# Kernel optimization log

Measured on AMD Instinct MI355X. Metric: run time of the kernel, lower is better.

Reference implementation:

```python
import jax, jax.numpy as jnp
import numpy as np

N, E, G = 25000, 400000, 8
D = 128  # node/edge/global feature width
CONCAT = 4 * D  # send + recv + edge + repeated-global


def _dense(k, fan_in, fan_out):
    kw, kb = jax.random.split(k)
    scale = 1.0 / np.sqrt(fan_in)
    W = jax.random.uniform(kw, (fan_in, fan_out), jnp.float32, -scale, scale)
    b = jax.random.uniform(kb, (fan_out,), jnp.float32, -scale, scale)
    return W, b


def setup_inputs() -> dict:
    key = jax.random.key(0)
    ks = jax.random.split(key, 16)
    nodes = jax.random.normal(ks[0], (N, D), jnp.float32)
    edges = jax.random.normal(ks[1], (E, D), jnp.float32)
    glbs = jax.random.normal(ks[2], (G, D), jnp.float32)
    senders = jax.random.randint(ks[3], (E,), 0, N, jnp.int32)
    receivers = jax.random.randint(ks[4], (E,), 0, N, jnp.int32)
    n_node = jnp.full((G,), N // G, jnp.int32)
    n_edge = jnpip = jnp.full((G,), E // G, jnp.int32)
    # node MLP [CONCAT -> 256 -> 128]
    Wn0, bn0 = _dense(ks[5], CONCAT, 256)
    Wn1, bn1 = _dense(ks[6], 256, 128)
    # edge MLP [CONCAT -> 256 -> 128]
    We0, be0 = _dense(ks[7], CONCAT, 256)
    We1, be1 = _dense(ks[8], 256, 128)
    # global MLPs [D -> 128] each, final [384 -> 128]
    Wgn, bgn = _dense(ks[9], D, 128)
    Wge, bge = _dense(ks[10], D, 128)
    Wg, bg = _dense(ks[11], D, 128)
    Wf, bf = _dense(ks[12], 3 * 128, 128)
    return dict(nodes=nodes, edges=edges, glbs=glbs, senders=senders,
                receivers=receivers, n_node=n_node, n_edge=n_edge,
                Wn0=Wn0, bn0=bn0, Wn1=Wn1, bn1=bn1,
                We0=We0, be0=be0, We1=We1, be1=be1,
                Wgn=Wgn, bgn=bgn, Wge=Wge, bge=bge,
                Wg=Wg, bg=bg, Wf=Wf, bf=bf)


def reference(nodes, edges, glbs, senders, receivers, n_node, n_edge,
              Wn0, bn0, Wn1, bn1, We0, be0, We1, be1,
              Wgn, bgn, Wge, bge, Wg, bg, Wf, bf):
    act = jax.nn.leaky_relu  # default negative_slope=0.01, dropout is identity

    def mlp2(x, W0, b0, W1, b1):
        return act(act(x @ W0 + b0) @ W1 + b1)

    def mlp1(x, W, b):
        return act(x @ W + b)

    # gather + concat: [E, 4D]
    edge_glb = jnp.repeat(glbs, n_edge, axis=0, total_repeat_length=E)
    concat = jnp.concatenate([nodes[senders], nodes[receivers], edges, edge_glb], axis=1)

    # per-edge node-message MLP, scatter-sum to receivers
    msgs = mlp2(concat, Wn0, bn0, Wn1, bn1)            # [E, 128]
    new_nodes = jax.ops.segment_sum(msgs, receivers, num_segments=N)

    # per-edge edge-update MLP
    new_edges = mlp2(concat, We0, be0, We1, be1)       # [E, 128]

    # per-graph sums of node/edge features (== split_and_sum)
    gid_n = jnp.repeat(jnp.arange(G), n_node, total_repeat_length=N)
    gid_e = jnp.repeat(jnp.arange(G), n_edge, total_repeat_length=E)
    sum_nodes = jax.ops.segment_sum(nodes, gid_n, num_segments=G)  # [G, D]
    sum_edges = jax.ops.segment_sum(edges, gid_e, num_segments=G)  # [G, D]

    tmp_g = mlp1(glbs, Wg, bg)
    tmp_n = mlp1(sum_nodes, Wgn, bgn)
    tmp_e = mlp1(sum_edges, Wge, bge)
    new_global = mlp1(jnp.concatenate([tmp_g, tmp_n, tmp_e], axis=1), Wf, bf)

    return new_nodes, new_edges, new_global
```

## Files before the change

kernel.cpp:

```cpp
#include <hip/hip_runtime.h>
#include <hip/hip_bf16.h>

#define D_ 128

typedef __attribute__((ext_vector_type(8))) short short8;
typedef __attribute__((ext_vector_type(4))) float f32x4;
typedef __attribute__((address_space(1))) const unsigned int g_u32;
typedef __attribute__((address_space(3))) unsigned int l_u32;

static __device__ __forceinline__ float lrelu(float x) { return x > 0.f ? x : 0.01f * x; }
static __device__ __forceinline__ short f2bf(float f) {
    __hip_bfloat16 h = __float2bfloat16(f);
    return *reinterpret_cast<short*>(&h);
}
static __device__ __forceinline__ unsigned short f2bfu(float f) {
    __hip_bfloat16 h = __float2bfloat16(f);
    return *reinterpret_cast<unsigned short*>(&h);
}
static __device__ __forceinline__ unsigned int f2fp8x4(float a, float b, float c, float d) {
    unsigned int p = __builtin_amdgcn_cvt_pk_fp8_f32(a, b, 0, 0);
    p = __builtin_amdgcn_cvt_pk_fp8_f32(c, d, p, 1);
    return p;
}

__global__ void prep(const float* __restrict__ Wn0, const float* __restrict__ We0,
                     const float* __restrict__ Wn1, const float* __restrict__ We1,
                     const float* __restrict__ bn0, const float* __restrict__ be0,
                     const float* __restrict__ bn1, const float* __restrict__ be1,
                     const float* __restrict__ nodes, const float* __restrict__ glbs,
                     long nq,
                     unsigned char* __restrict__ W0F, short* __restrict__ W1T,
                     float* __restrict__ b0c, float* __restrict__ b1c,
                     unsigned char* __restrict__ nodes_f8, unsigned char* __restrict__ glbs_f8) {
    long i = (long)blockIdx.x * 256 + threadIdx.x;
    if (i < nq) {
        float4 v = ((const float4*)nodes)[i];
        ((unsigned int*)nodes_f8)[i] = f2fp8x4(v.x, v.y, v.z, v.w);
        return;
    }
    long j = i - nq;
    if (j < 512 * 128) {
        int n = (int)(j >> 7), k4 = (int)(j & 127);
        float v0, v1, v2, v3;
        if (n < 256) {
            v0 = Wn0[(k4 * 4 + 0) * 256 + n]; v1 = Wn0[(k4 * 4 + 1) * 256 + n];
            v2 = Wn0[(k4 * 4 + 2) * 256 + n]; v3 = Wn0[(k4 * 4 + 3) * 256 + n];
        } else {
            int m = n - 256;
            v0 = We0[(k4 * 4 + 0) * 256 + m]; v1 = We0[(k4 * 4 + 1) * 256 + m];
            v2 = We0[(k4 * 4 + 2) * 256 + m]; v3 = We0[(k4 * 4 + 3) * 256 + m];
        }
        ((unsigned int*)W0F)[n * 128 + k4] = f2fp8x4(v0, v1, v2, v3);
        return;
    }
    j -= 512 * 128;
    if (j < 256 * 256) {
        int n = (int)(j >> 8), k = (int)(j & 255);
        float v = (n < 128) ? Wn1[k * 128 + n] : We1[k * 128 + (n - 128)];
        W1T[j] = f2bf(v);
        return;
    }
    j -= 256 * 256;
    if (j < 512) { b0c[j] = (j < 256) ? bn0[j] : be0[j - 256]; return; }
    if (j < 768) { int t = (int)j - 512; b1c[t] = (t < 128) ? bn1[t] : be1[t - 128]; return; }
    j -= 768;
    if (j < 256) {
        const float* g4 = glbs + j * 4;
        ((unsigned int*)glbs_f8)[j] = f2fp8x4(g4[0], g4[1], g4[2], g4[3]);
    }
}

__global__ void hist_recv(const int* __restrict__ receivers, int E_, int* __restrict__ cnt) {
    int e = blockIdx.x * 256 + threadIdx.x;
    if (e < E_) atomicAdd(&cnt[receivers[e]], 1);
}

__global__ void scan_counts(const int* __restrict__ cnt, int N_, int* __restrict__ off) {
    __shared__ int part[256];
    int t = threadIdx.x;
    int chunk = (N_ + 255) / 256;
    int b = t * chunk, e = min(N_, b + chunk);
    int s = 0;
    for (int i = b; i < e; i++) s += cnt[i];
    part[t] = s;
    __syncthreads();
    for (int o = 1; o < 256; o <<= 1) {
        int v = (t >= o) ? part[t - o] : 0;
        __syncthreads();
        part[t] += v;
        __syncthreads();
    }
    int run = part[t] - s;
    for (int i = b; i < e; i++) { off[i] = run; run += cnt[i]; }
}

__global__ void place_edges(const int* __restrict__ receivers, int E_,
                            int* __restrict__ off, int* __restrict__ sorted) {
    int e = blockIdx.x * 256 + threadIdx.x;
    if (e < E_) {
        int p = atomicAdd(&off[receivers[e]], 1);
        sorted[p] = e;
    }
}

__global__ void seg_sum(const float* __restrict__ src, const int* __restrict__ counts,
                        int G, int rows, int chunk, float* __restrict__ out) {
    int c4 = threadIdx.x & 31;
    int rl = threadIdx.x >> 5;
    int r0 = blockIdx.x * chunk + rl;
    int rend = min(rows, blockIdx.x * chunk + chunk);
    int s_ = 0;
    int cu0 = 0x7fffffff, cu1 = 0x7fffffff, cu2 = 0x7fffffff, cu3 = 0x7fffffff;
    int cu4 = 0x7fffffff, cu5 = 0x7fffffff, cu6 = 0x7fffffff, cu7 = 0x7fffffff;
#define CUF(I, CU) if (I < G) { s_ += counts[I]; CU = s_; }
    CUF(0, cu0) CUF(1, cu1) CUF(2, cu2) CUF(3, cu3)
    CUF(4, cu4) CUF(5, cu5) CUF(6, cu6) CUF(7, cu7)
#undef CUF
    f32x4 acc = {0.f, 0.f, 0.f, 0.f};
    int accg = -1;
    for (int r = r0; r < rend; r += 8) {
        int g = (r >= cu0) + (r >= cu1) + (r >= cu2) + (r >= cu3)
              + (r >= cu4) + (r >= cu5) + (r >= cu6) + (r >= cu7);
        if (g != accg) {
            if (accg >= 0) {
#pragma unroll
                for (int j = 0; j < 4; j++) atomicAdd(&out[accg * D_ + c4 * 4 + j], acc[j]);
            }
            acc = (f32x4){0.f, 0.f, 0.f, 0.f}; accg = g;
        }
        const float4 v = *(const float4*)(src + (long)r * D_ + c4 * 4);
        acc[0] += v.x; acc[1] += v.y; acc[2] += v.z; acc[3] += v.w;
    }
    if (accg >= 0) {
#pragma unroll
        for (int j = 0; j < 4; j++) atomicAdd(&out[accg * D_ + c4 * 4 + j], acc[j]);
    }
}

__global__ void conv_sum_edges(const float* __restrict__ src, const int* __restrict__ counts,
                               int G, int rows, int chunk,
                               float* __restrict__ out, unsigned char* __restrict__ dst_f8) {
    int c4 = threadIdx.x & 31;
    int rl = threadIdx.x >> 5;
    int r0 = blockIdx.x * chunk + rl;
    int rend = min(rows, blockIdx.x * chunk + chunk);
    int s_ = 0;
    int cu0 = 0x7fffffff, cu1 = 0x7fffffff, cu2 = 0x7fffffff, cu3 = 0x7fffffff;
    int cu4 = 0x7fffffff, cu5 = 0x7fffffff, cu6 = 0x7fffffff, cu7 = 0x7fffffff;
#define CUF(I, CU) if (I < G) { s_ += counts[I]; CU = s_; }
    CUF(0, cu0) CUF(1, cu1) CUF(2, cu2) CUF(3, cu3)
    CUF(4, cu4) CUF(5, cu5) CUF(6, cu6) CUF(7, cu7)
#undef CUF
    f32x4 acc = {0.f, 0.f, 0.f, 0.f};
    int accg = -1;
    for (int r = r0; r < rend; r += 8) {
        int g = (r >= cu0) + (r >= cu1) + (r >= cu2) + (r >= cu3)
              + (r >= cu4) + (r >= cu5) + (r >= cu6) + (r >= cu7);
        if (g != accg) {
            if (accg >= 0) {
#pragma unroll
                for (int j = 0; j < 4; j++) atomicAdd(&out[accg * D_ + c4 * 4 + j], acc[j]);
            }
            acc = (f32x4){0.f, 0.f, 0.f, 0.f}; accg = g;
        }
        const float4 v = *(const float4*)(src + (long)r * D_ + c4 * 4);
        acc[0] += v.x; acc[1] += v.y; acc[2] += v.z; acc[3] += v.w;
        ((unsigned int*)dst_f8)[(long)r * 32 + c4] = f2fp8x4(v.x, v.y, v.z, v.w);
    }
    if (accg >= 0) {
#pragma unroll
        for (int j = 0; j < 4; j++) atomicAdd(&out[accg * D_ + c4 * 4 + j], acc[j]);
    }
}

__global__ void global_mlp(const float* __restrict__ glbs, const float* __restrict__ sumn,
                           const float* __restrict__ sume,
                           const float* __restrict__ Wg, const float* __restrict__ bg,
                           const float* __restrict__ Wgn, const float* __restrict__ bgn,
                           const float* __restrict__ Wge, const float* __restrict__ bge,
                           const float* __restrict__ Wf, const float* __restrict__ bfv,
                           float* __restrict__ outg) {
    __shared__ float s_tmp[384];
    int r = blockIdx.x;
    int c = threadIdx.x;
    float a0 = 0.f, a1 = 0.f, a2 = 0.f;
    for (int k = 0; k < 128; k++) {
        a0 += glbs[r * 128 + k] * Wg[k * 128 + c];
        a1 += sumn[r * 128 + k] * Wgn[k * 128 + c];
        a2 += sume[r * 128 + k] * Wge[k * 128 + c];
    }
    s_tmp[c]       = lrelu(a0 + bg[c]);
    s_tmp[128 + c] = lrelu(a1 + bgn[c]);
    s_tmp[256 + c] = lrelu(a2 + bge[c]);
    __syncthreads();
    float a = 0.f;
    for (int k = 0; k < 384; k++) a += s_tmp[k] * Wf[k * 128 + c];
    outg[r * 128 + c] = lrelu(a + bfv[c]);
}

__launch_bounds__(512, 4)
__global__ void edge_mlp(const unsigned char* __restrict__ nodes_f8,
                         const unsigned char* __restrict__ edges_f8,
                         const unsigned char* __restrict__ glbs_f8,
                         const int* __restrict__ senders, const int* __restrict__ receivers,
                         const int* __restrict__ sorted_eid,
                         const int* __restrict__ n_edge, int G, int NT,
                         const unsigned char* __restrict__ W0F, const short* __restrict__ W1T,
                         const float* __restrict__ b0c, const float* __restrict__ b1c,
                         float* __restrict__ out_nodes, float* __restrict__ out_edges) {
    __shared__ __align__(16) char sX[65536];
    __shared__ int s_eid[64], s_recv[64], s_snd[64], s_gid[64];

    const int tid  = threadIdx.x;
    const int lane = tid & 63;
    const int wid  = tid >> 6;
    const int wn   = wid;
    const int l15  = lane & 15;
    const int lk   = lane >> 4;

    const int tile = blockIdx.x;
    const int base = tile * 64;

    int s_ = 0;
    int cu0 = 0x7fffffff, cu1 = 0x7fffffff, cu2 = 0x7fffffff, cu3 = 0x7fffffff;
    int cu4 = 0x7fffffff, cu5 = 0x7fffffff, cu6 = 0x7fffffff, cu7 = 0x7fffffff;
#define CUF(I, CU) if (I < G) { s_ += n_edge[I]; CU = s_; }
    CUF(0, cu0) CUF(1, cu1) CUF(2, cu2) CUF(3, cu3)
    CUF(4, cu4) CUF(5, cu5) CUF(6, cu6) CUF(7, cu7)
#undef CUF

    if (tid < 64) {
        int eid = sorted_eid[base + tid];
        s_eid[tid]  = eid;
        s_snd[tid]  = senders[eid];
        s_recv[tid] = receivers[eid];
        s_gid[tid]  = (eid >= cu0) + (eid >= cu1) + (eid >= cu2) + (eid >= cu3)
                    + (eid >= cu4) + (eid >= cu5) + (eid >= cu6) + (eid >= cu7);
    }
    __syncthreads();

#pragma unroll
    for (int r = 0; r < 4; ++r) {
        const int p   = r * 8 + wid;
        const int row = 2 * p + (lane >> 5);
        const int src = (lane >> 3) & 3;
        const int sub = lane & 7;
        char* dst = sX + p * 1024;
        const unsigned char* bp = (src == 0) ? nodes_f8 + (long)s_snd[row] * 128
                                 : (src == 1) ? nodes_f8 + (long)s_recv[row] * 128
                                 : (src == 2) ? edges_f8 + (long)s_eid[row] * 128
                                              : glbs_f8 + (long)s_gid[row] * 128;
        __builtin_amdgcn_global_load_lds((g_u32*)(bp + ((sub ^ (row & 7)) << 4)), (l_u32*)dst, 16, 0, 0);
    }
    __syncthreads();

    {
        f32x4 acc[4][2];
#pragma unroll
        for (int mt = 0; mt < 4; ++mt)
#pragma unroll
            for (int nt = 0; nt < 2; ++nt) acc[mt][nt] = (f32x4){0.f, 0.f, 0.f, 0.f};

#pragma unroll
        for (int t = 0; t < 16; ++t) {
            long bfr[2];
#pragma unroll
            for (int nt = 0; nt < 2; ++nt) {
                int n = wn * 32 + nt * 16 + l15;
                bfr[nt] = *(const long*)(W0F + (long)n * 512 + t * 32 + lk * 8);
            }
#pragma unroll
            for (int mt = 0; mt < 4; ++mt) {
                int row = mt * 16 + l15;
                int g16 = (t * 2 + (lk >> 1)) ^ (row & 7);
                long af = *(const long*)(sX + row * 512 + (g16 << 4) + ((lk & 1) << 3));
#pragma unroll
                for (int nt = 0; nt < 2; ++nt)
                    acc[mt][nt] = __builtin_amdgcn_mfma_f32_16x16x32_fp8_fp8(af, bfr[nt], acc[mt][nt], 0, 0, 0);
            }
        }
#pragma unroll
        for (int nt = 0; nt < 2; ++nt) {
            int col = wn * 32 + nt * 16 + l15;
            float bias = b0c[col];
#pragma unroll
            for (int mt = 0; mt < 4; ++mt) {
#pragma unroll
                for (int q = 0; q < 4; ++q) {
                    int row = mt * 16 + lk * 4 + q;
                    float v = lrelu(acc[mt][nt][q] + bias);
                    *(short*)(sX + 32768 + row * 512 + ((col * 2) ^ ((row & 7) << 4))) = f2bf(v);
                }
            }
        }
    }

    {
        f32x4 acc[4][2];
#pragma unroll
        for (int mt = 0; mt < 4; ++mt)
#pragma unroll
            for (int nt = 0; nt < 2; ++nt) acc[mt][nt] = (f32x4){0.f, 0.f, 0.f, 0.f};

#pragma unroll
        for (int t = 0; t < 16; ++t) {
            long bfr[2];
#pragma unroll
            for (int nt = 0; nt < 2; ++nt) {
                int n = 256 + wn * 32 + nt * 16 + l15;
                bfr[nt] = *(const long*)(W0F + (long)n * 512 + t * 32 + lk * 8);
            }
#pragma unroll
            for (int mt = 0; mt < 4; ++mt) {
                int row = mt * 16 + l15;
                int g16 = (t * 2 + (lk >> 1)) ^ (row & 7);
                long af = *(const long*)(sX + row * 512 + (g16 << 4) + ((lk & 1) << 3));
#pragma unroll
                for (int nt = 0; nt < 2; ++nt)
                    acc[mt][nt] = __builtin_amdgcn_mfma_f32_16x16x32_fp8_fp8(af, bfr[nt], acc[mt][nt], 0, 0, 0);
            }
        }
        __syncthreads();
#pragma unroll
        for (int nt = 0; nt < 2; ++nt) {
            int col = wn * 32 + nt * 16 + l15;
            float bias = b0c[256 + col];
#pragma unroll
            for (int mt = 0; mt < 4; ++mt) {
#pragma unroll
                for (int q = 0; q < 4; ++q) {
                    int row = mt * 16 + lk * 4 + q;
                    float v = lrelu(acc[mt][nt][q] + bias);
                    *(short*)(sX + row * 512 + ((col * 2) ^ ((row & 7) << 4))) = f2bf(v);
                }
            }
        }
    }
    __syncthreads();

    const int branch = wid >> 2;
    const int qn     = wid & 3;
    const int hreg   = branch ? 0 : 32768;
    f32x4 acc2[4][2];
#pragma unroll
    for (int mt = 0; mt < 4; ++mt)
#pragma unroll
        for (int nt = 0; nt < 2; ++nt) acc2[mt][nt] = (f32x4){0.f, 0.f, 0.f, 0.f};

#pragma unroll
    for (int kt = 0; kt < 8; ++kt) {
        short8 bfr2[2];
#pragma unroll
        for (int nt = 0; nt < 2; ++nt) {
            int ncl = qn * 32 + nt * 16 + l15;
            bfr2[nt] = *(const short8*)(W1T + (long)(branch * 128 + ncl) * 256 + kt * 32 + lk * 8);
        }
#pragma unroll
        for (int mt = 0; mt < 4; ++mt) {
            int row = mt * 16 + l15;
            int kbyte = kt * 64 + lk * 16;
            short8 af = *(const short8*)(sX + hreg + row * 512 + (kbyte ^ ((row & 7) << 4)));
#pragma unroll
            for (int nt = 0; nt < 2; ++nt)
                acc2[mt][nt] = __builtin_amdgcn_mfma_f32_16x16x32_bf16(af, bfr2[nt], acc2[mt][nt], 0, 0, 0);
        }
    }
    __syncthreads();

#pragma unroll
    for (int nt = 0; nt < 2; ++nt) {
        int ncl = qn * 32 + nt * 16 + l15;
        float bias = b1c[branch * 128 + ncl];
#pragma unroll
        for (int mt = 0; mt < 4; ++mt) {
#pragma unroll
            for (int q = 0; q < 4; ++q) {
                int row = mt * 16 + lk * 4 + q;
                float v = lrelu(acc2[mt][nt][q] + bias);
                if (branch == 0) {
                    *(float*)(sX + 32768 + row * 512 + ((ncl * 4) ^ (((row >> 2) & 3) << 6))) = v;
                } else {
                    out_edges[(long)s_eid[row] * D_ + ncl] = v;
                }
            }
        }
    }
    __syncthreads();

    {
        int c  = tid & 127;
        int qr = tid >> 7;
        int r0 = qr * 16;
        float v[16];
#pragma unroll
        for (int i = 0; i < 16; ++i) {
            int r = r0 + i;
            v[i] = *(const float*)(sX + 32768 + r * 512 + ((c * 4) ^ (((r >> 2) & 3) << 6)));
        }
        float acc_s = 0.f;
        int cur = s_recv[r0];
#pragma unroll
        for (int i = 0; i < 16; ++i) {
            int rc = s_recv[r0 + i];
            if (rc != cur) {
                atomicAdd(&out_nodes[(long)cur * D_ + c], acc_s);
                acc_s = 0.f; cur = rc;
            }
            acc_s += v[i];
        }
        atomicAdd(&out_nodes[(long)cur * D_ + c], acc_s);
    }
}

extern "C" void kernel_launch(void* const* d_in, const int* in_sizes, int n_in,
                              void* d_out, int out_size, void* d_ws, size_t ws_size,
                              hipStream_t stream) {
    const float* nodes     = (const float*)d_in[0];
    const float* edges     = (const float*)d_in[1];
    const float* glbs      = (const float*)d_in[2];
    const int*   senders   = (const int*)d_in[3];
    const int*   receivers = (const int*)d_in[4];
    const int*   n_node    = (const int*)d_in[5];
    const int*   n_edge    = (const int*)d_in[6];
    const float* Wn0 = (const float*)d_in[7];
    const float* bn0 = (const float*)d_in[8];
    const float* Wn1 = (const float*)d_in[9];
    const float* bn1 = (const float*)d_in[10];
    const float* We0 = (const float*)d_in[11];
    const float* be0 = (const float*)d_in[12];
    const float* We1 = (const float*)d_in[13];
    const float* be1 = (const float*)d_in[14];
    const float* Wgn = (const float*)d_in[15];
    const float* bgn = (const float*)d_in[16];
    const float* Wge = (const float*)d_in[17];
    const float* bge = (const float*)d_in[18];
    const float* Wg  = (const float*)d_in[19];
    const float* bg  = (const float*)d_in[20];
    const float* Wf  = (const float*)d_in[21];
    const float* bfv = (const float*)d_in[22];

    const int N = in_sizes[0] / 128;
    const int E = in_sizes[1] / 128;
    const int G = in_sizes[2] / 128;
    const int NT = E / 64;

    char* ws = (char*)d_ws;
    unsigned char* W0F = (unsigned char*)(ws);
    short* W1T  = (short*)(ws + 262144);
    float* b0c  = (float*)(ws + 393216);
    float* b1c  = (float*)(ws + 395264);
    float* sumn = (float*)(ws + 396288);
    float* sume = (float*)(ws + 400384);
    unsigned char* glbs_f8  = (unsigned char*)(ws + 404480);
    unsigned char* nodes_f8 = (unsigned char*)(ws + 405504);
    char* ws2 = ws + 405504 + (size_t)N * 128;
    int* cnt        = (int*)(ws2);
    int* tmp_off    = (int*)(ws2 + (size_t)N * 4);
    int* sorted_eid = (int*)(ws2 + (size_t)N * 8);
    unsigned char* edges_f8 = (unsigned char*)(ws2 + (size_t)N * 8 + (size_t)E * 4);

    float* out_nodes = (float*)d_out;
    float* out_edges = out_nodes + (long)N * 128;
    float* out_glb   = out_edges + (long)E * 128;

    hipMemsetAsync(out_nodes, 0, (size_t)N * 128 * sizeof(float), stream);
    hipMemsetAsync(sumn, 0, 8192, stream);
    hipMemsetAsync(cnt, 0, (size_t)N * 4, stream);

    const long nq = (long)N * 32;
    const long prep_items = nq + 512 * 128 + 256 * 256 + 768 + 256;
    prep<<<(int)((prep_items + 255) / 256), 256, 0, stream>>>(
        Wn0, We0, Wn1, We1, bn0, be0, bn1, be1, nodes, glbs, nq,
        W0F, W1T, b0c, b1c, nodes_f8, glbs_f8);

    hist_recv<<<(E + 255) / 256, 256, 0, stream>>>(receivers, E, cnt);
    scan_counts<<<1, 256, 0, stream>>>(cnt, N, tmp_off);
    place_edges<<<(E + 255) / 256, 256, 0, stream>>>(receivers, E, tmp_off, sorted_eid);

    conv_sum_edges<<<(E + 511) / 512, 256, 0, stream>>>(edges, n_edge, G, E, 512, sume, edges_f8);

    edge_mlp<<<NT, 512, 0, stream>>>(nodes_f8, edges_f8, glbs_f8, senders, receivers,
                                     sorted_eid, n_edge, G, NT,
                                     W0F, W1T, b0c, b1c, out_nodes, out_edges);

    seg_sum<<<(N + 127) / 128, 256, 0, stream>>>(nodes, n_node, G, N, 128, sumn);

    global_mlp<<<G, 128, 0, stream>>>(glbs, sumn, sume, Wg, bg, Wgn, bgn, Wge, bge, Wf, bfv,
                                      out_glb);
}
```

Measured before the change: 919.5 us.

## Fuse receiver histogram into edge conversion, use plain stores for owned segments, widen global MLP

Folds the receiver histogram atomics into the conv_sum_edges pass and drops the separate hist_recv launch. In edge_mlp, a receiver segment that lies wholly inside one thread's 16-row range now gets a plain store instead of an atomicAdd; neighbouring receivers are checked through shared values for the previous and next tile. global_mlp now runs its three small input MLPs in parallel on 384 threads. The plain-store path depends on out_nodes being zero-initialised and on receivers being sorted, so each receiver is fully owned by one range.

```diff
diff --git a/kernel.cpp b/kernel.cpp
--- a/kernel.cpp
+++ b/kernel.cpp
@@ -68,11 +68,6 @@
         const float* g4 = glbs + j * 4;
         ((unsigned int*)glbs_f8)[j] = f2fp8x4(g4[0], g4[1], g4[2], g4[3]);
     }
-}
-
-__global__ void hist_recv(const int* __restrict__ receivers, int E_, int* __restrict__ cnt) {
-    int e = blockIdx.x * 256 + threadIdx.x;
-    if (e < E_) atomicAdd(&cnt[receivers[e]], 1);
 }
 
 __global__ void scan_counts(const int* __restrict__ cnt, int N_, int* __restrict__ off) {
@@ -138,6 +133,7 @@
 }
 
 __global__ void conv_sum_edges(const float* __restrict__ src, const int* __restrict__ counts,
+                               const int* __restrict__ receivers, int* __restrict__ hist,
                                int G, int rows, int chunk,
                                float* __restrict__ out, unsigned char* __restrict__ dst_f8) {
     int c4 = threadIdx.x & 31;
@@ -166,6 +162,7 @@
         const float4 v = *(const float4*)(src + (long)r * D_ + c4 * 4);
         acc[0] += v.x; acc[1] += v.y; acc[2] += v.z; acc[3] += v.w;
         ((unsigned int*)dst_f8)[(long)r * 32 + c4] = f2fp8x4(v.x, v.y, v.z, v.w);
+        if (c4 == 0) atomicAdd(&hist[receivers[r]], 1);
     }
     if (accg >= 0) {
 #pragma unroll
@@ -182,20 +179,20 @@
                            float* __restrict__ outg) {
     __shared__ float s_tmp[384];
     int r = blockIdx.x;
-    int c = threadIdx.x;
-    float a0 = 0.f, a1 = 0.f, a2 = 0.f;
-    for (int k = 0; k < 128; k++) {
-        a0 += glbs[r * 128 + k] * Wg[k * 128 + c];
-        a1 += sumn[r * 128 + k] * Wgn[k * 128 + c];
-        a2 += sume[r * 128 + k] * Wge[k * 128 + c];
-    }
-    s_tmp[c]       = lrelu(a0 + bg[c]);
-    s_tmp[128 + c] = lrelu(a1 + bgn[c]);
-    s_tmp[256 + c] = lrelu(a2 + bge[c]);
-    __syncthreads();
+    int c   = threadIdx.x & 127;
+    int grp = threadIdx.x >> 7;
+    const float* src = (grp == 0) ? glbs : (grp == 1) ? sumn : sume;
+    const float* W   = (grp == 0) ? Wg   : (grp == 1) ? Wgn  : Wge;
+    const float* b   = (grp == 0) ? bg   : (grp == 1) ? bgn  : bge;
     float a = 0.f;
-    for (int k = 0; k < 384; k++) a += s_tmp[k] * Wf[k * 128 + c];
-    outg[r * 128 + c] = lrelu(a + bfv[c]);
+    for (int k = 0; k < 128; k++) a += src[r * 128 + k] * W[k * 128 + c];
+    s_tmp[grp * 128 + c] = lrelu(a + b[c]);
+    __syncthreads();
+    if (threadIdx.x < 128) {
+        float a2 = 0.f;
+        for (int k = 0; k < 384; k++) a2 += s_tmp[k] * Wf[k * 128 + c];
+        outg[r * 128 + c] = lrelu(a2 + bfv[c]);
+    }
 }
 
 __launch_bounds__(512, 4)
@@ -210,6 +207,7 @@
                          float* __restrict__ out_nodes, float* __restrict__ out_edges) {
     __shared__ __align__(16) char sX[65536];
     __shared__ int s_eid[64], s_recv[64], s_snd[64], s_gid[64];
+    __shared__ int sh_rprev, sh_rnext;
 
     const int tid  = threadIdx.x;
     const int lane = tid & 63;
@@ -220,6 +218,7 @@
 
     const int tile = blockIdx.x;
     const int base = tile * 64;
+    const int Etot = NT * 64;
 
     int s_ = 0;
     int cu0 = 0x7fffffff, cu1 = 0x7fffffff, cu2 = 0x7fffffff, cu3 = 0x7fffffff;
@@ -237,6 +236,8 @@
         s_gid[tid]  = (eid >= cu0) + (eid >= cu1) + (eid >= cu2) + (eid >= cu3)
                     + (eid >= cu4) + (eid >= cu5) + (eid >= cu6) + (eid >= cu7);
     }
+    if (tid == 64) sh_rprev = (base > 0) ? receivers[sorted_eid[base - 1]] : -1;
+    if (tid == 65) sh_rnext = (base + 64 < Etot) ? receivers[sorted_eid[base + 64]] : -1;
     __syncthreads();
 
 #pragma unroll
@@ -390,25 +391,30 @@
     {
         int c  = tid & 127;
         int qr = tid >> 7;
-        int r0 = qr * 16;
+        int r0 = qr * 16, r1 = r0 + 16;
         float v[16];
 #pragma unroll
         for (int i = 0; i < 16; ++i) {
             int r = r0 + i;
             v[i] = *(const float*)(sX + 32768 + r * 512 + ((c * 4) ^ (((r >> 2) & 3) << 6)));
         }
+        int leftr = (r0 == 0) ? sh_rprev : s_recv[r0 - 1];
         float acc_s = 0.f;
         int cur = s_recv[r0];
+        bool shl = (leftr == cur);
 #pragma unroll
         for (int i = 0; i < 16; ++i) {
             int rc = s_recv[r0 + i];
             if (rc != cur) {
-                atomicAdd(&out_nodes[(long)cur * D_ + c], acc_s);
-                acc_s = 0.f; cur = rc;
+                if (shl) atomicAdd(&out_nodes[(long)cur * D_ + c], acc_s);
+                else     out_nodes[(long)cur * D_ + c] = acc_s;
+                shl = false; acc_s = 0.f; cur = rc;
             }
             acc_s += v[i];
         }
-        atomicAdd(&out_nodes[(long)cur * D_ + c], acc_s);
+        int rightr = (r1 == 64) ? sh_rnext : s_recv[r1];
+        if (shl || rightr == cur) atomicAdd(&out_nodes[(long)cur * D_ + c], acc_s);
+        else                      out_nodes[(long)cur * D_ + c] = acc_s;
     }
 }
 
@@ -473,11 +479,11 @@
         Wn0, We0, Wn1, We1, bn0, be0, bn1, be1, nodes, glbs, nq,
         W0F, W1T, b0c, b1c, nodes_f8, glbs_f8);
 
-    hist_recv<<<(E + 255) / 256, 256, 0, stream>>>(receivers, E, cnt);
+    conv_sum_edges<<<(E + 511) / 512, 256, 0, stream>>>(edges, n_edge, receivers, cnt,
+                                                        G, E, 512, sume, edges_f8);
+
     scan_counts<<<1, 256, 0, stream>>>(cnt, N, tmp_off);
     place_edges<<<(E + 255) / 256, 256, 0, stream>>>(receivers, E, tmp_off, sorted_eid);
-
-    conv_sum_edges<<<(E + 511) / 512, 256, 0, stream>>>(edges, n_edge, G, E, 512, sume, edges_f8);
 
     edge_mlp<<<NT, 512, 0, stream>>>(nodes_f8, edges_f8, glbs_f8, senders, receivers,
                                      sorted_eid, n_edge, G, NT,
@@ -485,6 +491,6 @@
 
     seg_sum<<<(N + 127) / 128, 256, 0, stream>>>(nodes, n_node, G, N, 128, sumn);
 
-    global_mlp<<<G, 128, 0, stream>>>(glbs, sumn, sume, Wg, bg, Wgn, bgn, Wge, bge, Wf, bfv,
+    global_mlp<<<G, 384, 0, stream>>>(glbs, sumn, sume, Wg, bg, Wgn, bgn, Wge, bge, Wf, bfv,
                                       out_glb);
 }
```

Result: faster. 895.6 us (-2.6%).
